# Performance work log

Measured on AMD Instinct MI355X. Metric: run time of the kernel, lower is better.

The kernel has to match this reference:

```python
import jax, jax.numpy as jnp
import numpy as np

B = 2048   # batch
D = 1280   # backbone feature dim (hardcoded in module)
E = 8      # num_classes == number of expert heads
ALPHA = 0.1
EPS = 1e-5


def _bn(x, g, b, m, v):
    # BatchNorm1d in eval mode: running stats
    return (x - m) * jax.lax.rsqrt(v + EPS) * g + b


def _ln(x, g, b):
    mu = jnp.mean(x, axis=-1, keepdims=True)
    var = jnp.mean((x - mu) ** 2, axis=-1, keepdims=True)
    return (x - mu) * jax.lax.rsqrt(var + EPS) * g + b


@jax.custom_vjp
def _grad_reverse(x):
    return x

def _gr_fwd(x):
    return x, None

def _gr_bwd(_, g):
    return (-ALPHA * g,)

_grad_reverse.defvjp(_gr_fwd, _gr_bwd)


def setup_inputs() -> dict:
    key = jax.random.key(0)
    ks = iter(jax.random.split(key, 80))
    def w(*s):
        return jax.random.normal(next(ks), s, dtype=jnp.float32) * 0.02
    def u(*s):
        return jax.random.uniform(next(ks), s, dtype=jnp.float32) + 0.5
    inp = {"source": jax.random.normal(next(ks), (B, D), dtype=jnp.float32)}
    # bottleneck: Linear(1280,512)+BN+ReLU, Linear(512,256)+BN+ReLU
    inp.update(bw1=w(D, 512), bb1=jnp.zeros(512), bg1=jnp.ones(512), bbe1=jnp.zeros(512), bm1=w(512), bv1=u(512))
    inp.update(bw2=w(512, 256), bb2=jnp.zeros(256), bg2=jnp.ones(256), bbe2=jnp.zeros(256), bm2=w(256), bv2=u(256))
    # source_fc: Linear(256, E) + LogSoftmax
    inp.update(cw=w(256, E), cb=jnp.zeros(E))
    # domain classifier: 1280->1024->1024->512->2 with BN
    inp.update(dw1=w(D, 1024), db1=jnp.zeros(1024), dg1=jnp.ones(1024), dbe1=jnp.zeros(1024), dm1=w(1024), dv1=u(1024))
    inp.update(dw2=w(1024, 1024), db2=jnp.zeros(1024), dg2=jnp.ones(1024), dbe2=jnp.zeros(1024), dm2=w(1024), dv2=u(1024))
    inp.update(dw3=w(1024, 512), db3=jnp.zeros(512), dg3=jnp.ones(512), dbe3=jnp.zeros(512), dm3=w(512), dv3=u(512))
    inp.update(dw4=w(512, 2), db4=jnp.zeros(2))
    # E stacked expert MLPs: 1280->1024->1024->512->2 with LayerNorm
    inp.update(ew1=w(E, D, 1024), eb1=jnp.zeros((E, 1024)), eg1=jnp.ones((E, 1024)), ebe1=jnp.zeros((E, 1024)))
    inp.update(ew2=w(E, 1024, 1024), eb2=jnp.zeros((E, 1024)), eg2=jnp.ones((E, 1024)), ebe2=jnp.zeros((E, 1024)))
    inp.update(ew3=w(E, 1024, 512), eb3=jnp.zeros((E, 512)), eg3=jnp.ones((E, 512)), ebe3=jnp.zeros((E, 512)))
    inp.update(ew4=w(E, 512, 2), eb4=jnp.zeros((E, 2)))
    return inp


def reference(source, bw1, bb1, bg1, bbe1, bm1, bv1, bw2, bb2, bg2, bbe2, bm2, bv2, cw, cb,
              dw1, db1, dg1, dbe1, dm1, dv1, dw2, db2, dg2, dbe2, dm2, dv2,
              dw3, db3, dg3, dbe3, dm3, dv3, dw4, db4,
              ew1, eb1, eg1, ebe1, ew2, eb2, eg2, ebe2, ew3, eb3, eg3, ebe3, ew4, eb4):
    share = source  # sharedNet modeled as identity on extracted features
    # bottleneck + classifier head
    h = jax.nn.relu(_bn(share @ bw1 + bb1, bg1, bbe1, bm1, bv1))
    h = jax.nn.relu(_bn(h @ bw2 + bb2, bg2, bbe2, bm2, bv2))
    src = jax.nn.log_softmax(h @ cw + cb, axis=-1)            # [B, E]
    label = jnp.argmax(src, axis=-1)                          # routing labels (detached by argmax)
    # gradient-reversed features
    rev = _grad_reverse(share)
    # global domain classifier (dropout = identity in eval)
    d = jax.nn.relu(_bn(rev @ dw1 + db1, dg1, dbe1, dm1, dv1))
    d = jax.nn.relu(_bn(d @ dw2 + db2, dg2, dbe2, dm2, dv2))
    d = jax.nn.relu(_bn(d @ dw3 + db3, dg3, dbe3, dm3, dv3))
    dclf = jax.nn.log_softmax(d @ dw4 + db4, axis=-1)         # [B, 2]
    # per-class domain experts: dense all-expert compute + per-sample gather
    x = jax.nn.relu(_ln(jnp.einsum('bd,edh->beh', rev, ew1) + eb1[None], eg1[None], ebe1[None]))
    x = jax.nn.relu(_ln(jnp.einsum('beh,ehk->bek', x, ew2) + eb2[None], eg2[None], ebe2[None]))
    x = jax.nn.relu(_ln(jnp.einsum('beh,ehk->bek', x, ew3) + eb3[None], eg3[None], ebe3[None]))
    eo = jax.nn.log_softmax(jnp.einsum('beh,ehk->bek', x, ew4) + eb4[None], axis=-1)  # [B, E, 2]
    sout = jnp.take_along_axis(eo, label[:, None, None], axis=1)[:, 0, :]             # [B, 2]
    return (src, dclf, sout, share)
```

## Files before the change

kernel.cpp:

```cpp
#include <hip/hip_runtime.h>

typedef unsigned short u16;
typedef short s8v __attribute__((ext_vector_type(8)));
typedef float f4v __attribute__((ext_vector_type(4)));

#define AS1 __attribute__((address_space(1)))
#define AS3 __attribute__((address_space(3)))

__device__ __forceinline__ float bf2f(u16 u) {
    union { unsigned int i; float f; } x; x.i = ((unsigned int)u) << 16; return x.f;
}
__device__ __forceinline__ u16 f2bf(float f) {
    union { float f; unsigned int i; } x; x.f = f;
    unsigned int r = x.i + 0x7fffu + ((x.i >> 16) & 1u);
    return (u16)(r >> 16);
}

__device__ __forceinline__ void glds16(const u16* g, u16* l) {
    __builtin_amdgcn_global_load_lds((AS1 void*)(g), (AS3 void*)(l), 16, 0, 0);
}

__device__ __forceinline__ int swz(int row, int kq) {
    return row * 64 + ((((kq >> 3) ^ row) & 7) << 3);
}

__global__ __launch_bounds__(256) void convT2_k(const float* __restrict__ Wa,
        const float* __restrict__ Wb, int zSplit,
        u16* __restrict__ WT, int N, int K)
{
    const int z = blockIdx.z;
    const float* W = (z < zSplit) ? Wa + (size_t)z * K * N
                                  : Wb + (size_t)(z - zSplit) * K * N;
    WT += (size_t)z * K * N;
    const int n0 = blockIdx.x * 64, k0 = blockIdx.y * 64;
    __shared__ float t[64][65];
    const int r = threadIdx.x >> 2;
    const int c = (threadIdx.x & 3) << 4;
    const float* wp = W + (size_t)(k0 + r) * N + n0 + c;
    #pragma unroll
    for (int q = 0; q < 16; q += 4) {
        float4 f = *(const float4*)(wp + q);
        t[c + q + 0][r] = f.x; t[c + q + 1][r] = f.y;
        t[c + q + 2][r] = f.z; t[c + q + 3][r] = f.w;
    }
    __syncthreads();
    u16* op = WT + (size_t)(n0 + r) * K + k0 + c;
    #pragma unroll
    for (int q = 0; q < 16; q += 8) {
        s8v v;
        #pragma unroll
        for (int j = 0; j < 8; ++j) v[j] = (short)f2bf(t[r][c + q + j]);
        *(s8v*)(op + q) = v;
    }
}

__global__ __launch_bounds__(256) void conv_k(const float* __restrict__ in,
        u16* __restrict__ out, int n8)
{
    const int i = blockIdx.x * 256 + threadIdx.x;
    if (i >= n8) return;
    const float4 f0 = ((const float4*)in)[i * 2];
    const float4 f1 = ((const float4*)in)[i * 2 + 1];
    s8v v;
    v[0]=(short)f2bf(f0.x); v[1]=(short)f2bf(f0.y);
    v[2]=(short)f2bf(f0.z); v[3]=(short)f2bf(f0.w);
    v[4]=(short)f2bf(f1.x); v[5]=(short)f2bf(f1.y);
    v[6]=(short)f2bf(f1.z); v[7]=(short)f2bf(f1.w);
    ((s8v*)out)[i] = v;
}

__device__ __forceinline__ void stage_tile(u16* AsH, u16* BsH,
        const u16* ga, const u16* gb, int kk, int ldsq, int K)
{
    #pragma unroll
    for (int q = 0; q < 4; ++q) {
        glds16(ga + kk + (size_t)q * 32 * K, AsH + q * 2048 + ldsq);
        glds16(gb + kk + (size_t)q * 32 * K, BsH + q * 2048 + ldsq);
    }
}

template<int HASDOM>
__global__ __launch_bounds__(256) void gemm_bt128_k(
    const u16* __restrict__ A0, size_t aStrideZ,
    const u16* __restrict__ WT0,
    const float* __restrict__ ebias,
    const float* __restrict__ dbias, const float* __restrict__ dgam,
    const float* __restrict__ dbet,  const float* __restrict__ dmean,
    const float* __restrict__ dvar,  int zdom,
    u16* __restrict__ out0, int M, int N, int K)
{
    const int z = blockIdx.z;
    const u16* A  = A0  + (size_t)z * aStrideZ;
    const u16* WT = WT0 + (size_t)z * N * K;
    u16* out = out0 + (size_t)z * M * N;

    const int n0 = blockIdx.x * 128, m0 = blockIdx.y * 128;
    const int t = threadIdx.x;
    const int w = t >> 6, lane = t & 63;
    const int lq = lane >> 4, lr = lane & 15;
    const int wm = (w >> 1) * 64, wn = (w & 1) * 64;

    __shared__ __align__(16) u16 As[2 * 128 * 64];
    __shared__ __align__(16) u16 Bs[2 * 128 * 64];

    f4v acc[4][4] = {};

    const int schunk = ((t & 7) ^ ((t >> 3) & 7)) << 3;
    const u16* ga = A  + (size_t)(m0 + (t >> 3)) * K + schunk;
    const u16* gb = WT + (size_t)(n0 + (t >> 3)) * K + schunk;
    const int ldsq = w * 512;

    const int NT = K >> 6;
    int cur = 0;
    stage_tile(As, Bs, ga, gb, 0, ldsq, K);
    __syncthreads();

    for (int tk = 0; tk < NT; ++tk) {
        if (tk + 1 < NT)
            stage_tile(As + (cur ^ 1) * 8192, Bs + (cur ^ 1) * 8192,
                       ga, gb, (tk + 1) << 6, ldsq, K);
        const u16* Ah = As + cur * 8192;
        const u16* Bh = Bs + cur * 8192;
        __builtin_amdgcn_s_setprio(1);
        #pragma unroll
        for (int ks = 0; ks < 64; ks += 32) {
            const int kq = ks + (lq << 3);
            s8v a[4], b[4];
            #pragma unroll
            for (int i = 0; i < 4; ++i) a[i] = *(const s8v*)&Ah[swz(wm + i*16 + lr, kq)];
            #pragma unroll
            for (int j = 0; j < 4; ++j) b[j] = *(const s8v*)&Bh[swz(wn + j*16 + lr, kq)];
            #pragma unroll
            for (int i = 0; i < 4; ++i)
                #pragma unroll
                for (int j = 0; j < 4; ++j)
                    acc[i][j] = __builtin_amdgcn_mfma_f32_16x16x32_bf16(a[i], b[j], acc[i][j], 0, 0, 0);
        }
        __builtin_amdgcn_s_setprio(0);
        __syncthreads();
        cur ^= 1;
    }

    float scale[4], shift[4];
    const bool dom = HASDOM && (z == zdom);
    #pragma unroll
    for (int j = 0; j < 4; ++j) {
        const int c = n0 + wn + j * 16 + lr;
        if (dom) {
            const float s = dgam[c] / sqrtf(dvar[c] + 1e-5f);
            scale[j] = s;
            shift[j] = (dbias[c] - dmean[c]) * s + dbet[c];
        } else {
            scale[j] = 1.f;
            shift[j] = ebias[(size_t)z * N + c];
        }
    }
    const int r0 = lq << 2;
    #pragma unroll
    for (int i = 0; i < 4; ++i) {
        #pragma unroll
        for (int r = 0; r < 4; ++r) {
            const int grow = m0 + wm + i * 16 + r0 + r;
            u16* orow = out + (size_t)grow * N + n0 + wn + lr;
            #pragma unroll
            for (int j = 0; j < 4; ++j) {
                float y = fmaf(acc[i][j][r], scale[j], shift[j]);
                if (dom) y = fmaxf(y, 0.f);
                orow[j * 16] = f2bf(y);
            }
        }
    }
}

__global__ __launch_bounds__(256) void gemm_f32sk_k(
    const float* __restrict__ A, const float* __restrict__ W,
    float* __restrict__ out, int M, int N, int K, int Ks)
{
    const int n0 = blockIdx.x * 64, m0 = blockIdx.y * 64;
    const int kb = blockIdx.z * Ks;
    out += (size_t)blockIdx.z * M * N;
    const int tid = threadIdx.x;
    const int tx = tid & 15, ty = tid >> 4;
    __shared__ float As[64][65];
    __shared__ float Bs[64][64];
    float acc[4][4] = {};
    const int sr = tid >> 2;
    const int sc = (tid & 3) << 4;
    for (int kk = kb; kk < kb + Ks; kk += 64) {
        const float* ap = A + (size_t)(m0 + sr) * K + kk + sc;
        #pragma unroll
        for (int q = 0; q < 4; ++q) {
            float4 f = *(const float4*)(ap + q * 4);
            As[sr][sc + q*4 + 0] = f.x; As[sr][sc + q*4 + 1] = f.y;
            As[sr][sc + q*4 + 2] = f.z; As[sr][sc + q*4 + 3] = f.w;
        }
        const float* wp = W + (size_t)(kk + sr) * N + n0 + sc;
        #pragma unroll
        for (int q = 0; q < 4; ++q)
            *(float4*)&Bs[sr][sc + q*4] = *(const float4*)(wp + q * 4);
        __syncthreads();
        #pragma unroll 4
        for (int kq = 0; kq < 64; ++kq) {
            float a[4], bv[4];
            #pragma unroll
            for (int i = 0; i < 4; ++i) a[i] = As[ty*4 + i][kq];
            #pragma unroll
            for (int j = 0; j < 4; ++j) bv[j] = Bs[kq][tx*4 + j];
            #pragma unroll
            for (int i = 0; i < 4; ++i)
                #pragma unroll
                for (int j = 0; j < 4; ++j)
                    acc[i][j] = fmaf(a[i], bv[j], acc[i][j]);
        }
        __syncthreads();
    }
    #pragma unroll
    for (int j = 0; j < 4; ++j) {
        const int c = n0 + tx*4 + j;
        #pragma unroll
        for (int i = 0; i < 4; ++i)
            out[(size_t)(m0 + ty*4 + i) * N + c] = acc[i][j];
    }
}

__global__ __launch_bounds__(256) void bnpre_k(const float* __restrict__ g,
        const float* __restrict__ be, const float* __restrict__ bb,
        const float* __restrict__ m, const float* __restrict__ v,
        float* __restrict__ scs, float* __restrict__ shs, int N)
{
    const int k = blockIdx.x * 256 + threadIdx.x;
    if (k >= N) return;
    const float sc = g[k] / sqrtf(v[k] + 1e-5f);
    scs[k] = sc;
    shs[k] = (bb[k] - m[k]) * sc + be[k];
}

__global__ __launch_bounds__(256) void h2gemm_k(
    const float* __restrict__ hp, const float* __restrict__ scs,
    const float* __restrict__ shs, const float* __restrict__ bw2,
    float* __restrict__ out, int B)
{
    const int n0 = blockIdx.x * 64, m0 = blockIdx.y * 64;
    const int kb = blockIdx.z * 128;
    out += (size_t)blockIdx.z * B * 256;
    const size_t sl = (size_t)B * 512;
    const int tid = threadIdx.x;
    const int tx = tid & 15, ty = tid >> 4;
    __shared__ float As[64][65];
    __shared__ float Bs[64][64];
    float acc[4][4] = {};
    const int sr = tid >> 2;
    const int sc = (tid & 3) << 4;
    for (int kk = kb; kk < kb + 128; kk += 64) {
        const float* ap = hp + (size_t)(m0 + sr) * 512 + kk + sc;
        #pragma unroll
        for (int q = 0; q < 4; ++q) {
            const float4 f0 = *(const float4*)(ap + q * 4);
            const float4 f1 = *(const float4*)(ap + sl + q * 4);
            const float4 f2 = *(const float4*)(ap + 2 * sl + q * 4);
            const float4 f3 = *(const float4*)(ap + 3 * sl + q * 4);
            const float4 g = *(const float4*)(scs + kk + sc + q * 4);
            const float4 h = *(const float4*)(shs + kk + sc + q * 4);
            As[sr][sc + q*4 + 0] = fmaxf(fmaf(f0.x + f1.x + f2.x + f3.x, g.x, h.x), 0.f);
            As[sr][sc + q*4 + 1] = fmaxf(fmaf(f0.y + f1.y + f2.y + f3.y, g.y, h.y), 0.f);
            As[sr][sc + q*4 + 2] = fmaxf(fmaf(f0.z + f1.z + f2.z + f3.z, g.z, h.z), 0.f);
            As[sr][sc + q*4 + 3] = fmaxf(fmaf(f0.w + f1.w + f2.w + f3.w, g.w, h.w), 0.f);
        }
        const float* wp = bw2 + (size_t)(kk + sr) * 256 + n0 + sc;
        #pragma unroll
        for (int q = 0; q < 4; ++q)
            *(float4*)&Bs[sr][sc + q*4] = *(const float4*)(wp + q * 4);
        __syncthreads();
        #pragma unroll 4
        for (int kq = 0; kq < 64; ++kq) {
            float a[4], bv[4];
            #pragma unroll
            for (int i = 0; i < 4; ++i) a[i] = As[ty*4 + i][kq];
            #pragma unroll
            for (int j = 0; j < 4; ++j) bv[j] = Bs[kq][tx*4 + j];
            #pragma unroll
            for (int i = 0; i < 4; ++i)
                #pragma unroll
                for (int j = 0; j < 4; ++j)
                    acc[i][j] = fmaf(a[i], bv[j], acc[i][j]);
        }
        __syncthreads();
    }
    #pragma unroll
    for (int j = 0; j < 4; ++j) {
        const int c = n0 + tx*4 + j;
        #pragma unroll
        for (int i = 0; i < 4; ++i)
            out[(size_t)(m0 + ty*4 + i) * 256 + c] = acc[i][j];
    }
}

__global__ __launch_bounds__(256) void cls_k(
    const float* __restrict__ h2p,
    const float* __restrict__ bg2, const float* __restrict__ bbe2,
    const float* __restrict__ bb2, const float* __restrict__ bm2,
    const float* __restrict__ bv2,
    const float* __restrict__ cw,  const float* __restrict__ cb,
    float* __restrict__ out_src, int* __restrict__ label, int B)
{
    const int b = blockIdx.x * 4 + (threadIdx.x >> 6);
    const int lane = threadIdx.x & 63;
    const size_t sl = (size_t)B * 256;
    const float* hb = h2p + (size_t)b * 256 + lane * 4;
    const float4 v0 = *(const float4*)(hb);
    const float4 v1 = *(const float4*)(hb + sl);
    const float4 v2 = *(const float4*)(hb + 2 * sl);
    const float4 v3 = *(const float4*)(hb + 3 * sl);
    const float4 gv = ((const float4*)bg2)[lane];
    const float4 vv = ((const float4*)bv2)[lane];
    const float4 bbv = ((const float4*)bb2)[lane];
    const float4 bmv = ((const float4*)bm2)[lane];
    const float4 bev = ((const float4*)bbe2)[lane];
    float h[4];
    {
        const float s0 = gv.x / sqrtf(vv.x + 1e-5f);
        const float s1 = gv.y / sqrtf(vv.y + 1e-5f);
        const float s2 = gv.z / sqrtf(vv.z + 1e-5f);
        const float s3 = gv.w / sqrtf(vv.w + 1e-5f);
        h[0] = fmaxf(fmaf(v0.x + v1.x + v2.x + v3.x, s0, (bbv.x - bmv.x) * s0 + bev.x), 0.f);
        h[1] = fmaxf(fmaf(v0.y + v1.y + v2.y + v3.y, s1, (bbv.y - bmv.y) * s1 + bev.y), 0.f);
        h[2] = fmaxf(fmaf(v0.z + v1.z + v2.z + v3.z, s2, (bbv.z - bmv.z) * s2 + bev.z), 0.f);
        h[3] = fmaxf(fmaf(v0.w + v1.w + v2.w + v3.w, s3, (bbv.w - bmv.w) * s3 + bev.w), 0.f);
    }
    float p[8] = {};
    #pragma unroll
    for (int j = 0; j < 4; ++j) {
        const float4 c0 = ((const float4*)cw)[(lane * 4 + j) * 2];
        const float4 c1 = ((const float4*)cw)[(lane * 4 + j) * 2 + 1];
        p[0] = fmaf(h[j], c0.x, p[0]); p[1] = fmaf(h[j], c0.y, p[1]);
        p[2] = fmaf(h[j], c0.z, p[2]); p[3] = fmaf(h[j], c0.w, p[3]);
        p[4] = fmaf(h[j], c1.x, p[4]); p[5] = fmaf(h[j], c1.y, p[5]);
        p[6] = fmaf(h[j], c1.z, p[6]); p[7] = fmaf(h[j], c1.w, p[7]);
    }
    #pragma unroll
    for (int off = 32; off; off >>= 1)
        #pragma unroll
        for (int c = 0; c < 8; ++c) p[c] += __shfl_xor(p[c], off, 64);
    if (lane == 0) {
        float lg[8];
        #pragma unroll
        for (int c = 0; c < 8; ++c) lg[c] = p[c] + cb[c];
        float mx = lg[0]; int am = 0;
        #pragma unroll
        for (int c = 1; c < 8; ++c) if (lg[c] > mx) { mx = lg[c]; am = c; }
        float ssum = 0.f;
        #pragma unroll
        for (int c = 0; c < 8; ++c) ssum += expf(lg[c] - mx);
        const float lse = mx + logf(ssum);
        #pragma unroll
        for (int c = 0; c < 8; ++c) out_src[b * 8 + c] = lg[c] - lse;
        label[b] = am;
    }
}

template<int N>
__global__ __launch_bounds__(256) void ln_relu_k(u16* __restrict__ Y,
        const float* __restrict__ g, const float* __restrict__ bb)
{
    const int z = blockIdx.y;
    u16* y = Y + ((size_t)z * gridDim.x + blockIdx.x) * N;
    const float* gz = g  + (size_t)z * N;
    const float* bz = bb + (size_t)z * N;
    const int t = threadIdx.x;
    constexpr int C = N >> 8;
    float vals[C];
    if (C == 4) {
        ushort4 u = ((const ushort4*)y)[t];
        vals[0] = bf2f(u.x); vals[1] = bf2f(u.y);
        vals[2] = bf2f(u.z); vals[3] = bf2f(u.w);
    } else {
        ushort2 u = ((const ushort2*)y)[t];
        vals[0] = bf2f(u.x); vals[1] = bf2f(u.y);
    }
    float s = 0.f, sq = 0.f;
    #pragma unroll
    for (int i = 0; i < C; ++i) { s += vals[i]; sq += vals[i] * vals[i]; }
    #pragma unroll
    for (int off = 32; off; off >>= 1) {
        s  += __shfl_xor(s,  off, 64);
        sq += __shfl_xor(sq, off, 64);
    }
    __shared__ float rs[4], rq[4];
    if ((t & 63) == 0) { rs[t >> 6] = s; rq[t >> 6] = sq; }
    __syncthreads();
    s  = rs[0] + rs[1] + rs[2] + rs[3];
    sq = rq[0] + rq[1] + rq[2] + rq[3];
    const float inv = 1.f / (float)N;
    const float mu  = s * inv;
    const float var = sq * inv - mu * mu;
    const float rstd = rsqrtf(var + 1e-5f);
    if (C == 4) {
        float4 gv = ((const float4*)gz)[t];
        float4 bv = ((const float4*)bz)[t];
        ushort4 o;
        o.x = f2bf(fmaxf((vals[0] - mu) * rstd * gv.x + bv.x, 0.f));
        o.y = f2bf(fmaxf((vals[1] - mu) * rstd * gv.y + bv.y, 0.f));
        o.z = f2bf(fmaxf((vals[2] - mu) * rstd * gv.z + bv.z, 0.f));
        o.w = f2bf(fmaxf((vals[3] - mu) * rstd * gv.w + bv.w, 0.f));
        ((ushort4*)y)[t] = o;
    } else {
        float2 gv = ((const float2*)gz)[t];
        float2 bv = ((const float2*)bz)[t];
        ushort2 o;
        o.x = f2bf(fmaxf((vals[0] - mu) * rstd * gv.x + bv.x, 0.f));
        o.y = f2bf(fmaxf((vals[1] - mu) * rstd * gv.y + bv.y, 0.f));
        ((ushort2*)y)[t] = o;
    }
}

__global__ __launch_bounds__(64) void head2_k(const u16* __restrict__ X, size_t xsz,
        const float* __restrict__ W, size_t wsz,
        const float* __restrict__ bias, size_t bsz,
        int K, float* __restrict__ out, size_t osz)
{
    const int b = blockIdx.x, z = blockIdx.y;
    const int lane = threadIdx.x;
    const u16* x = X + z * xsz + (size_t)b * K;
    const float* Wz = W + z * wsz;
    const float* bz = bias + z * bsz;
    float* o = out + z * osz + (size_t)b * 2;
    float p0 = 0.f, p1 = 0.f;
    for (int k8 = lane; k8 < (K >> 3); k8 += 64) {
        const uint4 raw = ((const uint4*)x)[k8];
        const u16* pu = (const u16*)&raw;
        const float4 w0 = ((const float4*)Wz)[k8 * 4 + 0];
        const float4 w1 = ((const float4*)Wz)[k8 * 4 + 1];
        const float4 w2 = ((const float4*)Wz)[k8 * 4 + 2];
        const float4 w3 = ((const float4*)Wz)[k8 * 4 + 3];
        p0 = fmaf(bf2f(pu[0]), w0.x, p0); p1 = fmaf(bf2f(pu[0]), w0.y, p1);
        p0 = fmaf(bf2f(pu[1]), w0.z, p0); p1 = fmaf(bf2f(pu[1]), w0.w, p1);
        p0 = fmaf(bf2f(pu[2]), w1.x, p0); p1 = fmaf(bf2f(pu[2]), w1.y, p1);
        p0 = fmaf(bf2f(pu[3]), w1.z, p0); p1 = fmaf(bf2f(pu[3]), w1.w, p1);
        p0 = fmaf(bf2f(pu[4]), w2.x, p0); p1 = fmaf(bf2f(pu[4]), w2.y, p1);
        p0 = fmaf(bf2f(pu[5]), w2.z, p0); p1 = fmaf(bf2f(pu[5]), w2.w, p1);
        p0 = fmaf(bf2f(pu[6]), w3.x, p0); p1 = fmaf(bf2f(pu[6]), w3.y, p1);
        p0 = fmaf(bf2f(pu[7]), w3.z, p0); p1 = fmaf(bf2f(pu[7]), w3.w, p1);
    }
    #pragma unroll
    for (int off = 32; off; off >>= 1) {
        p0 += __shfl_xor(p0, off, 64);
        p1 += __shfl_xor(p1, off, 64);
    }
    if (lane == 0) {
        const float l0 = p0 + bz[0];
        const float l1 = p1 + bz[1];
        const float mx = fmaxf(l0, l1);
        const float lse = mx + logf(expf(l0 - mx) + expf(l1 - mx));
        o[0] = l0 - lse;
        o[1] = l1 - lse;
    }
}

__global__ __launch_bounds__(256) void gather_k(const float* __restrict__ eo,
        const int* __restrict__ label, float* __restrict__ out, int B)
{
    const int b = blockIdx.x * 256 + threadIdx.x;
    if (b >= B) return;
    const int e = label[b];
    out[b * 2]     = eo[((size_t)e * B + b) * 2];
    out[b * 2 + 1] = eo[((size_t)e * B + b) * 2 + 1];
}

__global__ __launch_bounds__(256) void copy16_k(const uint4* __restrict__ in,
                                                uint4* __restrict__ out, int n16)
{
    const int i = blockIdx.x * blockDim.x + threadIdx.x;
    if (i < n16) out[i] = in[i];
}


extern "C" void kernel_launch(void* const* d_in, const int* in_sizes, int n_in,
                              void* d_out, int out_size, void* d_ws, size_t ws_size,
                              hipStream_t stream)
{
    const int B = 2048, D = 1280, E = 8;

    const float* src = (const float*)d_in[0];
    const float *bw1 = (const float*)d_in[1],  *bb1 = (const float*)d_in[2],
                *bg1 = (const float*)d_in[3],  *bbe1 = (const float*)d_in[4],
                *bm1 = (const float*)d_in[5],  *bv1 = (const float*)d_in[6];
    const float *bw2 = (const float*)d_in[7],  *bb2 = (const float*)d_in[8],
                *bg2 = (const float*)d_in[9],  *bbe2 = (const float*)d_in[10],
                *bm2 = (const float*)d_in[11], *bv2 = (const float*)d_in[12];
    const float *cw  = (const float*)d_in[13], *cb  = (const float*)d_in[14];
    const float *dw1 = (const float*)d_in[15], *db1 = (const float*)d_in[16],
                *dg1 = (const float*)d_in[17], *dbe1 = (const float*)d_in[18],
                *dm1 = (const float*)d_in[19], *dv1 = (const float*)d_in[20];
    const float *dw2 = (const float*)d_in[21], *db2 = (const float*)d_in[22],
                *dg2 = (const float*)d_in[23], *dbe2 = (const float*)d_in[24],
                *dm2 = (const float*)d_in[25], *dv2 = (const float*)d_in[26];
    const float *dw3 = (const float*)d_in[27], *db3 = (const float*)d_in[28],
                *dg3 = (const float*)d_in[29], *dbe3 = (const float*)d_in[30],
                *dm3 = (const float*)d_in[31], *dv3 = (const float*)d_in[32];
    const float *dw4 = (const float*)d_in[33], *db4 = (const float*)d_in[34];
    const float *ew1 = (const float*)d_in[35], *eb1 = (const float*)d_in[36],
                *eg1 = (const float*)d_in[37], *ebe1 = (const float*)d_in[38];
    const float *ew2 = (const float*)d_in[39], *eb2 = (const float*)d_in[40],
                *eg2 = (const float*)d_in[41], *ebe2 = (const float*)d_in[42];
    const float *ew3 = (const float*)d_in[43], *eb3 = (const float*)d_in[44],
                *eg3 = (const float*)d_in[45], *ebe3 = (const float*)d_in[46];
    const float *ew4 = (const float*)d_in[47], *eb4 = (const float*)d_in[48];

    float* out_src   = (float*)d_out;
    float* out_dclf  = out_src + B * E;
    float* out_sout  = out_dclf + B * 2;
    float* out_share = out_sout + B * 2;

    char* ws = (char*)d_ws;
    u16*   wslot = (u16*)ws;
    u16*   srcb  = (u16*)(ws + 13107200);
    u16*   acta  = (u16*)(ws + 18350080);
    u16*   actb  = (u16*)(ws + 39321600);
    float* eo    = (float*)(ws + 60293120);
    int*   label = (int*)(ws + 60424192);
    float* hp    = (float*)(ws + 18350080);
    float* h2p   = (float*)(ws);
    float* scs   = (float*)(ws + 12582912);
    float* shs   = (float*)(ws + 12587008);

    const size_t s1024 = (size_t)B * 1024, s512 = (size_t)B * 512;

    conv_k<<<dim3(B * D / 8 / 256), 256, 0, stream>>>(src, srcb, B * D / 8);
    copy16_k<<<dim3(B * D * 4 / 16 / 256), 256, 0, stream>>>(
        (const uint4*)src, (uint4*)out_share, B * D * 4 / 16);

    bnpre_k<<<dim3(2), 256, 0, stream>>>(bg1, bbe1, bb1, bm1, bv1, scs, shs, 512);
    gemm_f32sk_k<<<dim3(512 / 64, B / 64, 4), 256, 0, stream>>>(
        src, bw1, hp, B, 512, D, 320);
    h2gemm_k<<<dim3(256 / 64, B / 64, 4), 256, 0, stream>>>(
        hp, scs, shs, bw2, h2p, B);
    cls_k<<<dim3(B / 4), 256, 0, stream>>>(
        h2p, bg2, bbe2, bb2, bm2, bv2, cw, cb, out_src, label, B);

    convT2_k<<<dim3(16, 20, 5), 256, 0, stream>>>(ew1, dw1, 4, wslot, 1024, 1280);
    gemm_bt128_k<1><<<dim3(8, 16, 5), 256, 0, stream>>>(
        srcb, 0, wslot, eb1, db1, dg1, dbe1, dm1, dv1, 4, acta, B, 1024, 1280);
    ln_relu_k<1024><<<dim3(B, 4), 256, 0, stream>>>(acta, eg1, ebe1);

    convT2_k<<<dim3(16, 16, 5), 256, 0, stream>>>(ew2, dw2, 4, wslot, 1024, 1024);
    gemm_bt128_k<1><<<dim3(8, 16, 5), 256, 0, stream>>>(
        acta, s1024, wslot, eb2, db2, dg2, dbe2, dm2, dv2, 4, actb, B, 1024, 1024);
    ln_relu_k<1024><<<dim3(B, 4), 256, 0, stream>>>(actb, eg2, ebe2);

    convT2_k<<<dim3(8, 16, 5), 256, 0, stream>>>(ew3, dw3, 4, wslot, 512, 1024);
    gemm_bt128_k<1><<<dim3(4, 16, 5), 256, 0, stream>>>(
        actb, s1024, wslot, eb3, db3, dg3, dbe3, dm3, dv3, 4, acta, B, 512, 1024);
    ln_relu_k<512><<<dim3(B, 4), 256, 0, stream>>>(acta, eg3, ebe3);

    head2_k<<<dim3(B, 4), 64, 0, stream>>>(
        acta, s512, ew4, 1024, eb4, 2, 512, eo, (size_t)B * 2);
    head2_k<<<dim3(B, 1), 64, 0, stream>>>(
        acta + (size_t)4 * B * 512, 0, dw4, 0, db4, 0, 512, out_dclf, 0);

    convT2_k<<<dim3(16, 20, 4), 256, 0, stream>>>(
        ew1 + (size_t)4*1280*1024, ew1 + (size_t)4*1280*1024, 4, wslot, 1024, 1280);
    gemm_bt128_k<0><<<dim3(8, 16, 4), 256, 0, stream>>>(
        srcb, 0, wslot, eb1 + (size_t)4*1024,
        nullptr, nullptr, nullptr, nullptr, nullptr, -1, acta, B, 1024, 1280);
    ln_relu_k<1024><<<dim3(B, 4), 256, 0, stream>>>(acta, eg1 + (size_t)4*1024, ebe1 + (size_t)4*1024);

    convT2_k<<<dim3(16, 16, 4), 256, 0, stream>>>(
        ew2 + (size_t)4*1024*1024, ew2 + (size_t)4*1024*1024, 4, wslot, 1024, 1024);
    gemm_bt128_k<0><<<dim3(8, 16, 4), 256, 0, stream>>>(
        acta, s1024, wslot, eb2 + (size_t)4*1024,
        nullptr, nullptr, nullptr, nullptr, nullptr, -1, actb, B, 1024, 1024);
    ln_relu_k<1024><<<dim3(B, 4), 256, 0, stream>>>(actb, eg2 + (size_t)4*1024, ebe2 + (size_t)4*1024);

    convT2_k<<<dim3(8, 16, 4), 256, 0, stream>>>(
        ew3 + (size_t)4*1024*512, ew3 + (size_t)4*1024*512, 4, wslot, 512, 1024);
    gemm_bt128_k<0><<<dim3(4, 16, 4), 256, 0, stream>>>(
        actb, s1024, wslot, eb3 + (size_t)4*512,
        nullptr, nullptr, nullptr, nullptr, nullptr, -1, acta, B, 512, 1024);
    ln_relu_k<512><<<dim3(B, 4), 256, 0, stream>>>(acta, eg3 + (size_t)4*512, ebe3 + (size_t)4*512);

    head2_k<<<dim3(B, 4), 64, 0, stream>>>(
        acta, s512, ew4 + (size_t)4*512*2, 1024, eb4 + 8, 2, 512,
        eo + (size_t)4 * B * 2, (size_t)B * 2);

    gather_k<<<dim3(B / 256), 256, 0, stream>>>(eo, label, out_sout, B);
}
```

Baseline: 582.8 us.

## Deepen GEMM prefetch, fuse small kernels, compute final LN and head only for routed expert

The bf16 MFMA GEMM now keeps two tiles in flight. It waits with an explicit vmcnt and raw barriers instead of a stage-then-syncthreads loop, so global-to-LDS loads overlap compute further ahead. The source bf16 conversion now also writes the share copy, and the BN scale/shift precompute is folded into h2gemm, which removes separate launches. The last expert LayerNorm, the 2-way head and the gather are replaced by one per-sample kernel that does LN plus head only for the routed expert, skipping the other experts' layer-3 LN and head work. This relies on hand-set vmcnt counts that match the number of loads each thread issues per stage.

```diff
diff --git a/kernel.cpp b/kernel.cpp
--- a/kernel.cpp
+++ b/kernel.cpp
@@ -54,8 +54,8 @@
     }
 }
 
-__global__ __launch_bounds__(256) void conv_k(const float* __restrict__ in,
-        u16* __restrict__ out, int n8)
+__global__ __launch_bounds__(256) void convsrc_k(const float* __restrict__ in,
+        u16* __restrict__ outb, float* __restrict__ outf, int n8)
 {
     const int i = blockIdx.x * 256 + threadIdx.x;
     if (i >= n8) return;
@@ -66,7 +66,9 @@
     v[2]=(short)f2bf(f0.z); v[3]=(short)f2bf(f0.w);
     v[4]=(short)f2bf(f1.x); v[5]=(short)f2bf(f1.y);
     v[6]=(short)f2bf(f1.z); v[7]=(short)f2bf(f1.w);
-    ((s8v*)out)[i] = v;
+    ((s8v*)outb)[i] = v;
+    ((float4*)outf)[i * 2]     = f0;
+    ((float4*)outf)[i * 2 + 1] = f1;
 }
 
 __device__ __forceinline__ void stage_tile(u16* AsH, u16* BsH,
@@ -111,16 +113,17 @@
     const int ldsq = w * 512;
 
     const int NT = K >> 6;
-    int cur = 0;
     stage_tile(As, Bs, ga, gb, 0, ldsq, K);
-    __syncthreads();
+    if (NT > 1) stage_tile(As + 8192, Bs + 8192, ga, gb, 64, ldsq, K);
 
     for (int tk = 0; tk < NT; ++tk) {
-        if (tk + 1 < NT)
-            stage_tile(As + (cur ^ 1) * 8192, Bs + (cur ^ 1) * 8192,
-                       ga, gb, (tk + 1) << 6, ldsq, K);
-        const u16* Ah = As + cur * 8192;
-        const u16* Bh = Bs + cur * 8192;
+        if (tk < NT - 1) asm volatile("s_waitcnt vmcnt(8)" ::: "memory");
+        else             asm volatile("s_waitcnt vmcnt(0)" ::: "memory");
+        __builtin_amdgcn_s_barrier();
+        __builtin_amdgcn_sched_barrier(0);
+
+        const u16* Ah = As + (tk & 1) * 8192;
+        const u16* Bh = Bs + (tk & 1) * 8192;
         __builtin_amdgcn_s_setprio(1);
         #pragma unroll
         for (int ks = 0; ks < 64; ks += 32) {
@@ -137,8 +140,12 @@
                     acc[i][j] = __builtin_amdgcn_mfma_f32_16x16x32_bf16(a[i], b[j], acc[i][j], 0, 0, 0);
         }
         __builtin_amdgcn_s_setprio(0);
-        __syncthreads();
-        cur ^= 1;
+        __builtin_amdgcn_sched_barrier(0);
+        __builtin_amdgcn_s_barrier();
+
+        if (tk + 2 < NT)
+            stage_tile(As + (tk & 1) * 8192, Bs + (tk & 1) * 8192,
+                       ga, gb, (tk + 2) << 6, ldsq, K);
     }
 
     float scale[4], shift[4];
@@ -223,21 +230,12 @@
     }
 }
 
-__global__ __launch_bounds__(256) void bnpre_k(const float* __restrict__ g,
-        const float* __restrict__ be, const float* __restrict__ bb,
-        const float* __restrict__ m, const float* __restrict__ v,
-        float* __restrict__ scs, float* __restrict__ shs, int N)
-{
-    const int k = blockIdx.x * 256 + threadIdx.x;
-    if (k >= N) return;
-    const float sc = g[k] / sqrtf(v[k] + 1e-5f);
-    scs[k] = sc;
-    shs[k] = (bb[k] - m[k]) * sc + be[k];
-}
-
 __global__ __launch_bounds__(256) void h2gemm_k(
-    const float* __restrict__ hp, const float* __restrict__ scs,
-    const float* __restrict__ shs, const float* __restrict__ bw2,
+    const float* __restrict__ hp,
+    const float* __restrict__ bg1, const float* __restrict__ bbe1,
+    const float* __restrict__ bb1, const float* __restrict__ bm1,
+    const float* __restrict__ bv1,
+    const float* __restrict__ bw2,
     float* __restrict__ out, int B)
 {
     const int n0 = blockIdx.x * 64, m0 = blockIdx.y * 64;
@@ -248,10 +246,19 @@
     const int tx = tid & 15, ty = tid >> 4;
     __shared__ float As[64][65];
     __shared__ float Bs[64][64];
+    __shared__ __align__(16) float scl[128], shl[128];
+    if (tid < 128) {
+        const int k = kb + tid;
+        const float sc = bg1[k] / sqrtf(bv1[k] + 1e-5f);
+        scl[tid] = sc;
+        shl[tid] = (bb1[k] - bm1[k]) * sc + bbe1[k];
+    }
+    __syncthreads();
     float acc[4][4] = {};
     const int sr = tid >> 2;
     const int sc = (tid & 3) << 4;
     for (int kk = kb; kk < kb + 128; kk += 64) {
+        const int kl = kk - kb;
         const float* ap = hp + (size_t)(m0 + sr) * 512 + kk + sc;
         #pragma unroll
         for (int q = 0; q < 4; ++q) {
@@ -259,8 +266,8 @@
             const float4 f1 = *(const float4*)(ap + sl + q * 4);
             const float4 f2 = *(const float4*)(ap + 2 * sl + q * 4);
             const float4 f3 = *(const float4*)(ap + 3 * sl + q * 4);
-            const float4 g = *(const float4*)(scs + kk + sc + q * 4);
-            const float4 h = *(const float4*)(shs + kk + sc + q * 4);
+            const float4 g = *(const float4*)&scl[kl + sc + q * 4];
+            const float4 h = *(const float4*)&shl[kl + sc + q * 4];
             As[sr][sc + q*4 + 0] = fmaxf(fmaf(f0.x + f1.x + f2.x + f3.x, g.x, h.x), 0.f);
             As[sr][sc + q*4 + 1] = fmaxf(fmaf(f0.y + f1.y + f2.y + f3.y, g.y, h.y), 0.f);
             As[sr][sc + q*4 + 2] = fmaxf(fmaf(f0.z + f1.z + f2.z + f3.z, g.z, h.z), 0.f);
@@ -369,14 +376,9 @@
     const int t = threadIdx.x;
     constexpr int C = N >> 8;
     float vals[C];
-    if (C == 4) {
-        ushort4 u = ((const ushort4*)y)[t];
-        vals[0] = bf2f(u.x); vals[1] = bf2f(u.y);
-        vals[2] = bf2f(u.z); vals[3] = bf2f(u.w);
-    } else {
-        ushort2 u = ((const ushort2*)y)[t];
-        vals[0] = bf2f(u.x); vals[1] = bf2f(u.y);
-    }
+    ushort4 u = ((const ushort4*)y)[t];
+    vals[0] = bf2f(u.x); vals[1] = bf2f(u.y);
+    vals[2] = bf2f(u.z); vals[3] = bf2f(u.w);
     float s = 0.f, sq = 0.f;
     #pragma unroll
     for (int i = 0; i < C; ++i) { s += vals[i]; sq += vals[i] * vals[i]; }
@@ -394,52 +396,64 @@
     const float mu  = s * inv;
     const float var = sq * inv - mu * mu;
     const float rstd = rsqrtf(var + 1e-5f);
-    if (C == 4) {
-        float4 gv = ((const float4*)gz)[t];
-        float4 bv = ((const float4*)bz)[t];
-        ushort4 o;
-        o.x = f2bf(fmaxf((vals[0] - mu) * rstd * gv.x + bv.x, 0.f));
-        o.y = f2bf(fmaxf((vals[1] - mu) * rstd * gv.y + bv.y, 0.f));
-        o.z = f2bf(fmaxf((vals[2] - mu) * rstd * gv.z + bv.z, 0.f));
-        o.w = f2bf(fmaxf((vals[3] - mu) * rstd * gv.w + bv.w, 0.f));
-        ((ushort4*)y)[t] = o;
-    } else {
-        float2 gv = ((const float2*)gz)[t];
-        float2 bv = ((const float2*)bz)[t];
-        ushort2 o;
-        o.x = f2bf(fmaxf((vals[0] - mu) * rstd * gv.x + bv.x, 0.f));
-        o.y = f2bf(fmaxf((vals[1] - mu) * rstd * gv.y + bv.y, 0.f));
-        ((ushort2*)y)[t] = o;
-    }
-}
-
-__global__ __launch_bounds__(64) void head2_k(const u16* __restrict__ X, size_t xsz,
-        const float* __restrict__ W, size_t wsz,
-        const float* __restrict__ bias, size_t bsz,
-        int K, float* __restrict__ out, size_t osz)
-{
-    const int b = blockIdx.x, z = blockIdx.y;
+    float4 gv = ((const float4*)gz)[t];
+    float4 bv = ((const float4*)bz)[t];
+    ushort4 o;
+    o.x = f2bf(fmaxf((vals[0] - mu) * rstd * gv.x + bv.x, 0.f));
+    o.y = f2bf(fmaxf((vals[1] - mu) * rstd * gv.y + bv.y, 0.f));
+    o.z = f2bf(fmaxf((vals[2] - mu) * rstd * gv.z + bv.z, 0.f));
+    o.w = f2bf(fmaxf((vals[3] - mu) * rstd * gv.w + bv.w, 0.f));
+    ((ushort4*)y)[t] = o;
+}
+
+__global__ __launch_bounds__(64) void headsel_k(
+    const u16* __restrict__ X,
+    const int* __restrict__ label,
+    const float* __restrict__ eg3, const float* __restrict__ ebe3,
+    const float* __restrict__ ew4, const float* __restrict__ eb4,
+    int zBase, float* __restrict__ out_sout, int B)
+{
+    const int b = blockIdx.x;
+    const int e = label[b];
+    if (e < zBase || e >= zBase + 4) return;
     const int lane = threadIdx.x;
-    const u16* x = X + z * xsz + (size_t)b * K;
-    const float* Wz = W + z * wsz;
-    const float* bz = bias + z * bsz;
-    float* o = out + z * osz + (size_t)b * 2;
+    const u16* x = X + ((size_t)(e - zBase) * B + b) * 512 + lane * 8;
+    uint4 raw = *(const uint4*)x;
+    const u16* pu = (const u16*)&raw;
+    float v[8];
+    #pragma unroll
+    for (int i = 0; i < 8; ++i) v[i] = bf2f(pu[i]);
+    float s = 0.f, sq = 0.f;
+    #pragma unroll
+    for (int i = 0; i < 8; ++i) { s += v[i]; sq += v[i] * v[i]; }
+    #pragma unroll
+    for (int off = 32; off; off >>= 1) {
+        s  += __shfl_xor(s,  off, 64);
+        sq += __shfl_xor(sq, off, 64);
+    }
+    const float mu = s * (1.f / 512.f);
+    const float var = sq * (1.f / 512.f) - mu * mu;
+    const float rstd = rsqrtf(var + 1e-5f);
+    const float* g  = eg3  + (size_t)e * 512 + lane * 8;
+    const float* be = ebe3 + (size_t)e * 512 + lane * 8;
+    const float4 g0 = *(const float4*)g,  g1 = *(const float4*)(g + 4);
+    const float4 b0 = *(const float4*)be, b1 = *(const float4*)(be + 4);
+    float h[8];
+    h[0] = fmaxf((v[0]-mu)*rstd*g0.x + b0.x, 0.f);
+    h[1] = fmaxf((v[1]-mu)*rstd*g0.y + b0.y, 0.f);
+    h[2] = fmaxf((v[2]-mu)*rstd*g0.z + b0.z, 0.f);
+    h[3] = fmaxf((v[3]-mu)*rstd*g0.w + b0.w, 0.f);
+    h[4] = fmaxf((v[4]-mu)*rstd*g1.x + b1.x, 0.f);
+    h[5] = fmaxf((v[5]-mu)*rstd*g1.y + b1.y, 0.f);
+    h[6] = fmaxf((v[6]-mu)*rstd*g1.z + b1.z, 0.f);
+    h[7] = fmaxf((v[7]-mu)*rstd*g1.w + b1.w, 0.f);
+    const float* W = ew4 + (size_t)e * 1024 + lane * 16;
     float p0 = 0.f, p1 = 0.f;
-    for (int k8 = lane; k8 < (K >> 3); k8 += 64) {
-        const uint4 raw = ((const uint4*)x)[k8];
-        const u16* pu = (const u16*)&raw;
-        const float4 w0 = ((const float4*)Wz)[k8 * 4 + 0];
-        const float4 w1 = ((const float4*)Wz)[k8 * 4 + 1];
-        const float4 w2 = ((const float4*)Wz)[k8 * 4 + 2];
-        const float4 w3 = ((const float4*)Wz)[k8 * 4 + 3];
-        p0 = fmaf(bf2f(pu[0]), w0.x, p0); p1 = fmaf(bf2f(pu[0]), w0.y, p1);
-        p0 = fmaf(bf2f(pu[1]), w0.z, p0); p1 = fmaf(bf2f(pu[1]), w0.w, p1);
-        p0 = fmaf(bf2f(pu[2]), w1.x, p0); p1 = fmaf(bf2f(pu[2]), w1.y, p1);
-        p0 = fmaf(bf2f(pu[3]), w1.z, p0); p1 = fmaf(bf2f(pu[3]), w1.w, p1);
-        p0 = fmaf(bf2f(pu[4]), w2.x, p0); p1 = fmaf(bf2f(pu[4]), w2.y, p1);
-        p0 = fmaf(bf2f(pu[5]), w2.z, p0); p1 = fmaf(bf2f(pu[5]), w2.w, p1);
-        p0 = fmaf(bf2f(pu[6]), w3.x, p0); p1 = fmaf(bf2f(pu[6]), w3.y, p1);
-        p0 = fmaf(bf2f(pu[7]), w3.z, p0); p1 = fmaf(bf2f(pu[7]), w3.w, p1);
+    #pragma unroll
+    for (int q = 0; q < 4; ++q) {
+        const float4 wv = *(const float4*)(W + q * 4);
+        p0 = fmaf(h[q*2],   wv.x, p0); p1 = fmaf(h[q*2],   wv.y, p1);
+        p0 = fmaf(h[q*2+1], wv.z, p0); p1 = fmaf(h[q*2+1], wv.w, p1);
     }
     #pragma unroll
     for (int off = 32; off; off >>= 1) {
@@ -447,30 +461,45 @@
         p1 += __shfl_xor(p1, off, 64);
     }
     if (lane == 0) {
-        const float l0 = p0 + bz[0];
-        const float l1 = p1 + bz[1];
+        const float l0 = p0 + eb4[e * 2];
+        const float l1 = p1 + eb4[e * 2 + 1];
         const float mx = fmaxf(l0, l1);
         const float lse = mx + logf(expf(l0 - mx) + expf(l1 - mx));
-        o[0] = l0 - lse;
-        o[1] = l1 - lse;
-    }
-}
-
-__global__ __launch_bounds__(256) void gather_k(const float* __restrict__ eo,
-        const int* __restrict__ label, float* __restrict__ out, int B)
-{
-    const int b = blockIdx.x * 256 + threadIdx.x;
-    if (b >= B) return;
-    const int e = label[b];
-    out[b * 2]     = eo[((size_t)e * B + b) * 2];
-    out[b * 2 + 1] = eo[((size_t)e * B + b) * 2 + 1];
-}
-
-__global__ __launch_bounds__(256) void copy16_k(const uint4* __restrict__ in,
-                                                uint4* __restrict__ out, int n16)
-{
-    const int i = blockIdx.x * blockDim.x + threadIdx.x;
-    if (i < n16) out[i] = in[i];
+        out_sout[b * 2]     = l0 - lse;
+        out_sout[b * 2 + 1] = l1 - lse;
+    }
+}
+
+__global__ __launch_bounds__(64) void head2_k(const u16* __restrict__ X,
+        const float* __restrict__ W, const float* __restrict__ bias,
+        float* __restrict__ out)
+{
+    const int b = blockIdx.x;
+    const int lane = threadIdx.x;
+    const u16* x = X + (size_t)b * 512 + lane * 8;
+    uint4 raw = *(const uint4*)x;
+    const u16* pu = (const u16*)&raw;
+    const float* Wz = W + lane * 16;
+    float p0 = 0.f, p1 = 0.f;
+    #pragma unroll
+    for (int q = 0; q < 4; ++q) {
+        const float4 wv = *(const float4*)(Wz + q * 4);
+        p0 = fmaf(bf2f(pu[q*2]),   wv.x, p0); p1 = fmaf(bf2f(pu[q*2]),   wv.y, p1);
+        p0 = fmaf(bf2f(pu[q*2+1]), wv.z, p0); p1 = fmaf(bf2f(pu[q*2+1]), wv.w, p1);
+    }
+    #pragma unroll
+    for (int off = 32; off; off >>= 1) {
+        p0 += __shfl_xor(p0, off, 64);
+        p1 += __shfl_xor(p1, off, 64);
+    }
+    if (lane == 0) {
+        const float l0 = p0 + bias[0];
+        const float l1 = p1 + bias[1];
+        const float mx = fmaxf(l0, l1);
+        const float lse = mx + logf(expf(l0 - mx) + expf(l1 - mx));
+        out[b * 2]     = l0 - lse;
+        out[b * 2 + 1] = l1 - lse;
+    }
 }
 
 
@@ -516,24 +545,18 @@
     u16*   srcb  = (u16*)(ws + 13107200);
     u16*   acta  = (u16*)(ws + 18350080);
     u16*   actb  = (u16*)(ws + 39321600);
-    float* eo    = (float*)(ws + 60293120);
-    int*   label = (int*)(ws + 60424192);
+    int*   label = (int*)(ws + 60293120);
     float* hp    = (float*)(ws + 18350080);
     float* h2p   = (float*)(ws);
-    float* scs   = (float*)(ws + 12582912);
-    float* shs   = (float*)(ws + 12587008);
 
     const size_t s1024 = (size_t)B * 1024, s512 = (size_t)B * 512;
 
-    conv_k<<<dim3(B * D / 8 / 256), 256, 0, stream>>>(src, srcb, B * D / 8);
-    copy16_k<<<dim3(B * D * 4 / 16 / 256), 256, 0, stream>>>(
-        (const uint4*)src, (uint4*)out_share, B * D * 4 / 16);
-
-    bnpre_k<<<dim3(2), 256, 0, stream>>>(bg1, bbe1, bb1, bm1, bv1, scs, shs, 512);
+    convsrc_k<<<dim3(B * D / 8 / 256), 256, 0, stream>>>(src, srcb, out_share, B * D / 8);
+
     gemm_f32sk_k<<<dim3(512 / 64, B / 64, 4), 256, 0, stream>>>(
         src, bw1, hp, B, 512, D, 320);
     h2gemm_k<<<dim3(256 / 64, B / 64, 4), 256, 0, stream>>>(
-        hp, scs, shs, bw2, h2p, B);
+        hp, bg1, bbe1, bb1, bm1, bv1, bw2, h2p, B);
     cls_k<<<dim3(B / 4), 256, 0, stream>>>(
         h2p, bg2, bbe2, bb2, bm2, bv2, cw, cb, out_src, label, B);
 
@@ -550,12 +573,11 @@
     convT2_k<<<dim3(8, 16, 5), 256, 0, stream>>>(ew3, dw3, 4, wslot, 512, 1024);
     gemm_bt128_k<1><<<dim3(4, 16, 5), 256, 0, stream>>>(
         actb, s1024, wslot, eb3, db3, dg3, dbe3, dm3, dv3, 4, acta, B, 512, 1024);
-    ln_relu_k<512><<<dim3(B, 4), 256, 0, stream>>>(acta, eg3, ebe3);
-
-    head2_k<<<dim3(B, 4), 64, 0, stream>>>(
-        acta, s512, ew4, 1024, eb4, 2, 512, eo, (size_t)B * 2);
-    head2_k<<<dim3(B, 1), 64, 0, stream>>>(
-        acta + (size_t)4 * B * 512, 0, dw4, 0, db4, 0, 512, out_dclf, 0);
+
+    headsel_k<<<dim3(B), 64, 0, stream>>>(
+        acta, label, eg3, ebe3, ew4, eb4, 0, out_sout, B);
+    head2_k<<<dim3(B), 64, 0, stream>>>(
+        acta + (size_t)4 * s512, dw4, db4, out_dclf);
 
     convT2_k<<<dim3(16, 20, 4), 256, 0, stream>>>(
         ew1 + (size_t)4*1280*1024, ew1 + (size_t)4*1280*1024, 4, wslot, 1024, 1280);
@@ -576,11 +598,7 @@
     gemm_bt128_k<0><<<dim3(4, 16, 4), 256, 0, stream>>>(
         actb, s1024, wslot, eb3 + (size_t)4*512,
         nullptr, nullptr, nullptr, nullptr, nullptr, -1, acta, B, 512, 1024);
-    ln_relu_k<512><<<dim3(B, 4), 256, 0, stream>>>(acta, eg3 + (size_t)4*512, ebe3 + (size_t)4*512);
-
-    head2_k<<<dim3(B, 4), 64, 0, stream>>>(
-        acta, s512, ew4 + (size_t)4*512*2, 1024, eb4 + 8, 2, 512,
-        eo + (size_t)4 * B * 2, (size_t)B * 2);
-
-    gather_k<<<dim3(B / 256), 256, 0, stream>>>(eo, label, out_sout, B);
-}
+
+    headsel_k<<<dim3(B), 64, 0, stream>>>(
+        acta, label, eg3, ebe3, ew4, eb4, 4, out_sout, B);
+}
```

Measured after the change: 552.4 us. 1.06x faster.
